# Performance work log

Hardware: AMD Instinct MI355X
Metric: run time of the kernel (lower is better)

The kernel has to match this reference:

```python
import jax, jax.numpy as jnp
import numpy as np

B, T, D, H = 4, 2048, 1024, 16
DK = D // H  # 64


def setup_inputs() -> dict:
    key = jax.random.key(0)
    ks = jax.random.split(key, 7)
    s = 1.0 / np.sqrt(D)
    x = jax.random.normal(ks[0], (B, T, D), dtype=jnp.float32)
    W_qkv = jax.random.normal(ks[1], (D, 3 * D), dtype=jnp.float32) * s
    b_qkv = jnp.zeros((3 * D,), dtype=jnp.float32)
    W_out = jax.random.normal(ks[2], (D, D), dtype=jnp.float32) * s
    b_out = jnp.zeros((D,), dtype=jnp.float32)
    # rotary tables: standard inv-freq construction, shape [T, DK//2]
    inv_freq = 1.0 / (10000.0 ** (np.arange(0, DK, 2, dtype=np.float32) / DK))
    ang = jnp.asarray(np.arange(T, dtype=np.float32)[:, None] * inv_freq[None, :])
    cos = jnp.cos(ang)
    sin = jnp.sin(ang)
    return {"x": x, "W_qkv": W_qkv, "b_qkv": b_qkv, "W_out": W_out,
            "b_out": b_out, "cos": cos, "sin": sin}


def _rope(t, cos, sin):
    # t: [B, H, T, DK]; cos/sin: [T, DK//2] broadcast over B, H
    t1, t2 = t[..., ::2], t[..., 1::2]
    return jnp.concatenate([t1 * cos - t2 * sin, t1 * sin + t2 * cos], axis=-1)


def reference(x, W_qkv, b_qkv, W_out, b_out, cos, sin):
    Bx, Tx, C = x.shape
    dk = C // H
    qkv = (x @ W_qkv + b_qkv).reshape(Bx, Tx, H, 3 * dk).transpose(0, 2, 1, 3)
    q, k, v = jnp.split(qkv, 3, axis=-1)  # each [B, H, T, dk]
    q = _rope(q, cos, sin)
    k = _rope(k, cos, sin)
    scores = jnp.einsum("bhtd,bhsd->bhts", q, k) / jnp.sqrt(jnp.float32(dk))
    causal = jnp.tril(jnp.ones((Tx, Tx), dtype=bool))  # [T, T]
    scores = jnp.where(causal, scores, jnp.float32(-jnp.inf))
    w = jax.nn.softmax(scores, axis=-1)  # dropout p=0.0 (eval): identity
    attn = jnp.einsum("bhts,bhsd->bhtd", w, v)
    attn = attn.transpose(0, 2, 1, 3).reshape(Bx, Tx, C)
    return attn @ W_out + b_out
```

## Files before the change

### kernel.cpp

```cpp
#include <hip/hip_runtime.h>
#include <cmath>

typedef __attribute__((ext_vector_type(4))) float f32x4;
typedef __attribute__((ext_vector_type(16))) float f32x16;
typedef __attribute__((ext_vector_type(8))) __bf16 bf16x8;
typedef __attribute__((ext_vector_type(8))) short s16x8;
typedef __attribute__((ext_vector_type(2))) unsigned int u32x2;

#define CB 4
#define CT 2048
#define CD 1024
#define CH 16
#define CDK 64
#define CBT 8192
#define CBH 64

#define GLOAD_LDS16(g, l)                                              \
  __builtin_amdgcn_global_load_lds(                                    \
      (const __attribute__((address_space(1))) unsigned int*)(g),      \
      (__attribute__((address_space(3))) unsigned int*)(l), 16, 0, 0)

__device__ __forceinline__ unsigned short f2bf(float f) {
  union { float f; unsigned u; } x; x.f = f;
  unsigned r = x.u + 0x7fffu + ((x.u >> 16) & 1u);
  return (unsigned short)(r >> 16);
}
__device__ __forceinline__ float bf2f(unsigned short b) {
  union { unsigned u; float f; } x; x.u = ((unsigned)b) << 16;
  return x.f;
}
__device__ __forceinline__ f32x4 mfma16(bf16x8 a, bf16x8 b, f32x4 c) {
  return __builtin_amdgcn_mfma_f32_16x16x32_bf16(a, b, c, 0, 0, 0);
}
__device__ __forceinline__ f32x16 mfma32(bf16x8 a, bf16x8 b, f32x16 c) {
  return __builtin_amdgcn_mfma_f32_32x32x16_bf16(a, b, c, 0, 0, 0);
}
__device__ __forceinline__ unsigned cvtpk(float lo, float hi) {
  unsigned r;
  asm("v_cvt_pk_bf16_f32 %0, %1, %2" : "=v"(r) : "v"(lo), "v"(hi));
  return r;
}

__global__ void convert_f32_bf16(const float* __restrict__ src,
                                 unsigned short* __restrict__ dst, int n) {
  int i = (blockIdx.x * blockDim.x + threadIdx.x) * 4;
  if (i >= n) return;
  float4 v = *(const float4*)(src + i);
  ushort4 o;
  o.x = f2bf(v.x); o.y = f2bf(v.y); o.z = f2bf(v.z); o.w = f2bf(v.w);
  *(ushort4*)(dst + i) = o;
}

__global__ void transpose_f32_bf16(const float* __restrict__ src,
                                   unsigned short* __restrict__ dst,
                                   int R, int C) {
  __shared__ float tile[32][33];
  const int x = threadIdx.x, y0 = threadIdx.y;
  const int ct = blockIdx.x, rt = blockIdx.y;
#pragma unroll
  for (int k = 0; k < 4; ++k) {
    int r = rt * 32 + y0 + k * 8;
    tile[y0 + k * 8][x] = src[(size_t)r * C + ct * 32 + x];
  }
  __syncthreads();
#pragma unroll
  for (int k = 0; k < 4; ++k) {
    int c = ct * 32 + y0 + k * 8;
    dst[(size_t)c * R + rt * 32 + x] = f2bf(tile[x][y0 + k * 8]);
  }
}

template <int MODE>
__global__ __launch_bounds__(256, 3) void gemm_bt(
    const unsigned short* __restrict__ A, const unsigned short* __restrict__ Bt,
    const float* __restrict__ bias, unsigned short* __restrict__ o0,
    unsigned short* __restrict__ o1, unsigned short* __restrict__ o2,
    float* __restrict__ fout, const float* __restrict__ cosT,
    const float* __restrict__ sinT, int M, int N, int K) {
  __shared__ __align__(16) unsigned short As[128 * 64];
  __shared__ __align__(16) unsigned short Bs[128 * 64];
  const int tid = threadIdx.x;
  const int lane = tid & 63, wid = tid >> 6;
  const int wr = wid >> 1, wc = wid & 1;
  const int m0 = blockIdx.x * 128, n0 = blockIdx.y * 128;
  const int l15 = lane & 15, l4 = lane >> 4;
  const int rx = l15 & 7;

  f32x4 acc[4][4];
#pragma unroll
  for (int i = 0; i < 4; ++i)
#pragma unroll
    for (int j = 0; j < 4; ++j) acc[i][j] = (f32x4){0.f, 0.f, 0.f, 0.f};

  const int srow = tid >> 3;
  const int scol = ((tid & 7) ^ (srow & 7)) * 8;
  const unsigned short* ag = A + (size_t)(m0 + srow) * K + scol;
  const unsigned short* bg = Bt + (size_t)(n0 + srow) * K + scol;
  unsigned short* asd = As + wid * 512;
  unsigned short* bsd = Bs + wid * 512;

  for (int k0 = 0; k0 < K; k0 += 64) {
#pragma unroll
    for (int p = 0; p < 4; ++p) {
      GLOAD_LDS16(ag + (size_t)(p * 32) * K + k0, asd + p * 2048);
      GLOAD_LDS16(bg + (size_t)(p * 32) * K + k0, bsd + p * 2048);
    }
    __syncthreads();
#pragma unroll
    for (int kk = 0; kk < 2; ++kk) {
      const int gsw = ((kk * 4 + l4) ^ rx) * 8;
      bf16x8 af[4], bfr[4];
#pragma unroll
      for (int i = 0; i < 4; ++i)
        af[i] = *(const bf16x8*)(&As[(wr * 64 + i * 16 + l15) * 64 + gsw]);
#pragma unroll
      for (int j = 0; j < 4; ++j)
        bfr[j] = *(const bf16x8*)(&Bs[(wc * 64 + j * 16 + l15) * 64 + gsw]);
#pragma unroll
      for (int i = 0; i < 4; ++i)
#pragma unroll
        for (int j = 0; j < 4; ++j)
          acc[i][j] = mfma16(af[i], bfr[j], acc[i][j]);
    }
    __syncthreads();
  }

  if (MODE == 1) {
#pragma unroll
    for (int i = 0; i < 4; ++i)
#pragma unroll
      for (int j = 0; j < 4; ++j) {
        const int row0 = m0 + wr * 64 + i * 16 + l4 * 4;
        const int col = n0 + wc * 64 + j * 16 + l15;
        const float bv = bias[col];
#pragma unroll
        for (int r = 0; r < 4; ++r)
          fout[(size_t)(row0 + r) * N + col] = acc[i][j][r] + bv;
      }
  } else {
#pragma unroll
    for (int i = 0; i < 4; ++i)
#pragma unroll
      for (int j = 0; j < 4; ++j) {
        const int col = n0 + wc * 64 + j * 16 + l15;
        const float bv = bias[col];
        const int h = col / 192;
        const int c = col % 192;
        const int sel = c >> 6;
        const int d = c & 63;
        if (sel < 2) {
          const int p = d >> 1;
          const bool even = (d & 1) == 0;
          const float qsc = (sel == 0) ? 0.18033688011112042592f : 1.0f;
          unsigned short* dst = (sel == 0) ? o0 : o1;
          const int dout = even ? p : (p + 32);
#pragma unroll
          for (int r = 0; r < 4; ++r) {
            const int row = m0 + wr * 64 + i * 16 + l4 * 4 + r;
            const int b = row >> 11, t = row & 2047;
            const float v = acc[i][j][r] + bv;
            const float vp = __shfl_xor(v, 1);
            const float cs = cosT[t * 32 + p];
            const float sn = sinT[t * 32 + p];
            const float ve = even ? v : vp;
            const float vo = even ? vp : v;
            const float res = (even ? (ve * cs - vo * sn)
                                    : (ve * sn + vo * cs)) * qsc;
            dst[((size_t)((b * CH + h) * CT + t)) * CDK + dout] = f2bf(res);
          }
        } else {
#pragma unroll
          for (int r = 0; r < 4; ++r) {
            const int row = m0 + wr * 64 + i * 16 + l4 * 4 + r;
            const int b = row >> 11, t = row & 2047;
            o2[((size_t)((b * CH + h) * CDK + d)) * CT + t] =
                f2bf(acc[i][j][r] + bv);
          }
        }
      }
  }
}

__global__ __launch_bounds__(256, 3) void attn_fwd4(
    const unsigned short* __restrict__ qg, const unsigned short* __restrict__ kg,
    const unsigned short* __restrict__ vtg, unsigned short* __restrict__ ctx) {
  __shared__ __align__(16) unsigned short Ks[3][64 * 64];
  __shared__ __align__(16) unsigned short Vt[3][64 * 64];
  const int tid = threadIdx.x, lane = tid & 63, w = tid >> 6;
  const int l31 = lane & 31, hi = lane >> 5;
  const int b1 = blockIdx.x;
  const int g8 = b1 & 7, idx8 = b1 >> 3;
  const int qb = 15 - (idx8 & 15);
  const int bh = g8 + 8 * (idx8 >> 4);
  const unsigned short* qp = qg + ((size_t)bh * CT + qb * 128) * CDK;
  const unsigned short* kp = kg + (size_t)bh * CT * CDK;
  const unsigned short* vp = vtg + (size_t)bh * CDK * CT;

  bf16x8 qf[4];
  {
    const unsigned short* qrow = qp + (size_t)(w * 32 + l31) * CDK + hi * 8;
#pragma unroll
    for (int ks = 0; ks < 4; ++ks) qf[ks] = *(const bf16x8*)(qrow + ks * 16);
  }
#pragma unroll
  for (int ks = 0; ks < 4; ++ks)
    asm volatile("" :: "v"(*(const f32x4*)&qf[ks]));

  const int lr = lane >> 3;
  const int gsw = ((lane & 7) ^ lr) * 8;
  const int row0 = w * 8 + lr;
  const unsigned short* ksrc0 = kp + (size_t)row0 * CDK + gsw;
  const unsigned short* ksrc1 = kp + (size_t)(row0 + 32) * CDK + gsw;
  const unsigned short* vsrc0 = vp + (size_t)row0 * CT + gsw;
  const unsigned short* vsrc1 = vp + (size_t)(row0 + 32) * CT + gsw;
  const int ld0 = w * 8 * 64;
  const int ld1 = (w * 8 + 32) * 64;

  const int NJ = 2 * qb + 2;
  const int njw = ((qb * 128 + w * 32 + 31) >> 6) + 1;
  const int qrow_g = qb * 128 + w * 32 + l31;

  auto STAGE = [&](int t, int buf) {
    const size_t koff = (size_t)t * 64 * CDK;
    const size_t voff = (size_t)t * 64;
    GLOAD_LDS16(ksrc0 + koff, &Ks[buf][ld0]);
    GLOAD_LDS16(ksrc1 + koff, &Ks[buf][ld1]);
    GLOAD_LDS16(vsrc0 + voff, &Vt[buf][ld0]);
    GLOAD_LDS16(vsrc1 + voff, &Vt[buf][ld1]);
  };

  f32x16 oacc[2];
#pragma unroll
  for (int nb = 0; nb < 2; ++nb)
#pragma unroll
    for (int r = 0; r < 16; ++r) oacc[nb][r] = 0.f;
  float lsum = 0.f;

  STAGE(0, 0);
  STAGE(1, 1);

  int b0 = 0;
  for (int j = 0; j < NJ; ++j) {
    int bp = b0 + 2; if (bp > 2) bp -= 3;
    if (j + 2 < NJ) STAGE(j + 2, bp);
    const int pend = NJ - 1 - j;
    if (pend >= 2)      asm volatile("s_waitcnt vmcnt(8)" ::: "memory");
    else if (pend == 1) asm volatile("s_waitcnt vmcnt(4)" ::: "memory");
    else                asm volatile("s_waitcnt vmcnt(0)" ::: "memory");
    __builtin_amdgcn_s_barrier();

    if (j < njw) {
      const unsigned short* KB = &Ks[b0][0];
      const unsigned short* VB = &Vt[b0][0];

      f32x16 pacc[2];
      __builtin_amdgcn_s_setprio(1);
#pragma unroll
      for (int kb = 0; kb < 2; ++kb) {
#pragma unroll
        for (int r = 0; r < 16; ++r) pacc[kb][r] = 0.f;
#pragma unroll
        for (int ks = 0; ks < 4; ++ks) {
          const int row = kb * 32 + l31;
          bf16x8 kf = *(const bf16x8*)(KB + row * 64 + (((ks * 2 + hi) ^ (row & 7)) * 8));
          pacc[kb] = mfma32(kf, qf[ks], pacc[kb]);
        }
      }
      __builtin_amdgcn_s_setprio(0);

      if (j == njw - 1) {
        const int key0 = j * 64;
#pragma unroll
        for (int kb = 0; kb < 2; ++kb)
#pragma unroll
          for (int r = 0; r < 16; ++r) {
            const int key = key0 + kb * 32 + (r & 3) + 8 * (r >> 2) + 4 * hi;
            if (key > qrow_g) pacc[kb][r] = -1e30f;
          }
      }

#pragma unroll
      for (int kb = 0; kb < 2; ++kb)
#pragma unroll
        for (int r = 0; r < 16; ++r)
          pacc[kb][r] = __builtin_amdgcn_exp2f(pacc[kb][r]);
      float rs;
      {
        float t[16];
#pragma unroll
        for (int r = 0; r < 16; ++r) t[r] = pacc[0][r] + pacc[1][r];
#pragma unroll
        for (int s = 8; s > 0; s >>= 1)
#pragma unroll
          for (int r = 0; r < s; ++r) t[r] += t[r + s];
        rs = t[0];
      }
      {
        unsigned ru = __float_as_uint(rs);
        u32x2 sw = __builtin_amdgcn_permlane32_swap(ru, ru, false, false);
        rs += __uint_as_float(hi ? sw[0] : sw[1]);
      }
      lsum += rs;

      bf16x8 pf[4];
#pragma unroll
      for (int kb = 0; kb < 2; ++kb)
#pragma unroll
        for (int half = 0; half < 2; ++half) {
          const int b0i = half * 8;
          unsigned c0 = cvtpk(pacc[kb][b0i + 0], pacc[kb][b0i + 1]);
          unsigned c1 = cvtpk(pacc[kb][b0i + 2], pacc[kb][b0i + 3]);
          unsigned c2 = cvtpk(pacc[kb][b0i + 4], pacc[kb][b0i + 5]);
          unsigned c3 = cvtpk(pacc[kb][b0i + 6], pacc[kb][b0i + 7]);
          u32x2 r02 = __builtin_amdgcn_permlane32_swap(c0, c2, false, false);
          u32x2 r13 = __builtin_amdgcn_permlane32_swap(c1, c3, false, false);
          union { unsigned u[4]; bf16x8 v; } fr;
          fr.u[0] = r02[0]; fr.u[1] = r13[0]; fr.u[2] = r02[1]; fr.u[3] = r13[1];
          pf[kb * 2 + half] = fr.v;
        }

      __builtin_amdgcn_s_setprio(1);
#pragma unroll
      for (int nb = 0; nb < 2; ++nb)
#pragma unroll
        for (int ks = 0; ks < 4; ++ks) {
          const int row = nb * 32 + l31;
          bf16x8 vf = *(const bf16x8*)(VB + row * 64 + (((ks * 2 + hi) ^ (row & 7)) * 8));
          oacc[nb] = mfma32(vf, pf[ks], oacc[nb]);
        }
      __builtin_amdgcn_s_setprio(0);
    }

    __builtin_amdgcn_s_barrier();
    b0 = (b0 == 2) ? 0 : b0 + 1;
  }

  __syncthreads();

  unsigned short* tr = &Ks[0][0] + w * 2048;
  const float inv = 1.f / lsum;
#pragma unroll
  for (int nb = 0; nb < 2; ++nb)
#pragma unroll
    for (int rp = 0; rp < 8; ++rp) {
      const int r = rp * 2;
      unsigned pkd = cvtpk(oacc[nb][r] * inv, oacc[nb][r + 1] * inv);
      const int d = nb * 32 + (r & 3) + 8 * (r >> 2) + 4 * hi;
      const int g = (d >> 3) ^ (l31 & 7);
      *(unsigned*)(tr + l31 * 64 + g * 8 + (d & 7)) = pkd;
    }
  const int b = bh >> 4, h = bh & 15;
#pragma unroll
  for (int s = 0; s < 4; ++s) {
    const int c = s * 64 + lane;
    const int qr = c >> 3, g = c & 7;
    s16x8 row = *(const s16x8*)(tr + qr * 64 + ((g ^ (qr & 7))) * 8);
    const int tok = qb * 128 + w * 32 + qr;
    *(s16x8*)(ctx + ((size_t)(b * CT + tok)) * CD + h * CDK + g * 8) = row;
  }
}

extern "C" void kernel_launch(void* const* d_in, const int* in_sizes, int n_in,
                              void* d_out, int out_size, void* d_ws, size_t ws_size,
                              hipStream_t stream) {
  (void)in_sizes; (void)n_in; (void)out_size; (void)ws_size;
  const float* x     = (const float*)d_in[0];
  const float* W_qkv = (const float*)d_in[1];
  const float* b_qkv = (const float*)d_in[2];
  const float* W_out = (const float*)d_in[3];
  const float* b_out = (const float*)d_in[4];
  const float* cosT  = (const float*)d_in[5];
  const float* sinT  = (const float*)d_in[6];
  float* out = (float*)d_out;

  unsigned short* xb   = (unsigned short*)d_ws;
  unsigned short* wqt  = xb + (size_t)CBT * CD;
  unsigned short* wot  = wqt + (size_t)3 * CD * CD;
  unsigned short* qbuf = wot + (size_t)CD * CD;
  unsigned short* kbuf = qbuf + (size_t)CBH * CT * CDK;
  unsigned short* vbuf = kbuf + (size_t)CBH * CT * CDK;
  unsigned short* ctx  = vbuf + (size_t)CBH * CT * CDK;

  {
    int n = CBT * CD;
    convert_f32_bf16<<<n / (256 * 4), 256, 0, stream>>>(x, xb, n);
  }
  transpose_f32_bf16<<<dim3(3 * CD / 32, CD / 32), dim3(32, 8), 0, stream>>>(
      W_qkv, wqt, CD, 3 * CD);
  transpose_f32_bf16<<<dim3(CD / 32, CD / 32), dim3(32, 8), 0, stream>>>(
      W_out, wot, CD, CD);
  gemm_bt<0><<<dim3(CBT / 128, 3 * CD / 128), 256, 0, stream>>>(
      xb, wqt, b_qkv, qbuf, kbuf, vbuf, nullptr, cosT, sinT, CBT, 3 * CD, CD);
  attn_fwd4<<<dim3(1024), 256, 0, stream>>>(qbuf, kbuf, vbuf, ctx);
  gemm_bt<1><<<dim3(CBT / 128, CD / 128), 256, 0, stream>>>(
      ctx, wot, b_out, nullptr, nullptr, nullptr, out, nullptr, nullptr,
      CBT, CD, CD);
}
```

Measured before the change: 172.8 us.

## Widen attention blocks to 256 query rows with 8 waves sharing K/V tiles

The attention kernel now runs 512 threads (8 waves) per block covering 256 query rows, so each staged 64-key K/V tile in LDS serves twice as many queries. Each thread issues one K and one V async load per stage instead of two each, and the vmcnt waits are halved to match. This cuts global K/V traffic and staging instructions per query. In exchange there are half as many blocks, the launch bound asks for 4 blocks/CU, and causal imbalance within a block grows, since early waves sit idle while later waves finish the diagonal tiles.

New measurement: 171.2 us. No clear change (-1.0%).

```diff
diff --git a/kernel.cpp b/kernel.cpp
--- a/kernel.cpp
+++ b/kernel.cpp
@@ -181,18 +181,19 @@
   }
 }
 
-__global__ __launch_bounds__(256, 3) void attn_fwd4(
+__global__ __launch_bounds__(512, 4) void attn_fwd5(
     const unsigned short* __restrict__ qg, const unsigned short* __restrict__ kg,
     const unsigned short* __restrict__ vtg, unsigned short* __restrict__ ctx) {
-  __shared__ __align__(16) unsigned short Ks[3][64 * 64];
-  __shared__ __align__(16) unsigned short Vt[3][64 * 64];
+  __shared__ __align__(16) unsigned short smem[24576];
+  unsigned short* Ks = smem;
+  unsigned short* Vt = smem + 12288;
   const int tid = threadIdx.x, lane = tid & 63, w = tid >> 6;
   const int l31 = lane & 31, hi = lane >> 5;
   const int b1 = blockIdx.x;
   const int g8 = b1 & 7, idx8 = b1 >> 3;
-  const int qb = 15 - (idx8 & 15);
-  const int bh = g8 + 8 * (idx8 >> 4);
-  const unsigned short* qp = qg + ((size_t)bh * CT + qb * 128) * CDK;
+  const int qb = 7 - (idx8 & 7);
+  const int bh = g8 + 8 * (idx8 >> 3);
+  const unsigned short* qp = qg + ((size_t)bh * CT + qb * 256) * CDK;
   const unsigned short* kp = kg + (size_t)bh * CT * CDK;
   const unsigned short* vp = vtg + (size_t)bh * CDK * CT;
 
@@ -207,26 +208,19 @@
     asm volatile("" :: "v"(*(const f32x4*)&qf[ks]));
 
   const int lr = lane >> 3;
+  const int srow = w * 8 + lr;
   const int gsw = ((lane & 7) ^ lr) * 8;
-  const int row0 = w * 8 + lr;
-  const unsigned short* ksrc0 = kp + (size_t)row0 * CDK + gsw;
-  const unsigned short* ksrc1 = kp + (size_t)(row0 + 32) * CDK + gsw;
-  const unsigned short* vsrc0 = vp + (size_t)row0 * CT + gsw;
-  const unsigned short* vsrc1 = vp + (size_t)(row0 + 32) * CT + gsw;
-  const int ld0 = w * 8 * 64;
-  const int ld1 = (w * 8 + 32) * 64;
-
-  const int NJ = 2 * qb + 2;
-  const int njw = ((qb * 128 + w * 32 + 31) >> 6) + 1;
-  const int qrow_g = qb * 128 + w * 32 + l31;
+  const unsigned short* ksrc = kp + (size_t)srow * CDK + gsw;
+  const unsigned short* vsrc = vp + (size_t)srow * CT + gsw;
+  const int ldo = w * 512;
+
+  const int NJ = 4 * qb + 4;
+  const int njw = ((qb * 256 + w * 32 + 31) >> 6) + 1;
+  const int qrow_g = qb * 256 + w * 32 + l31;
 
   auto STAGE = [&](int t, int buf) {
-    const size_t koff = (size_t)t * 64 * CDK;
-    const size_t voff = (size_t)t * 64;
-    GLOAD_LDS16(ksrc0 + koff, &Ks[buf][ld0]);
-    GLOAD_LDS16(ksrc1 + koff, &Ks[buf][ld1]);
-    GLOAD_LDS16(vsrc0 + voff, &Vt[buf][ld0]);
-    GLOAD_LDS16(vsrc1 + voff, &Vt[buf][ld1]);
+    GLOAD_LDS16(ksrc + (size_t)t * 64 * CDK, Ks + buf * 4096 + ldo);
+    GLOAD_LDS16(vsrc + (size_t)t * 64, Vt + buf * 4096 + ldo);
   };
 
   f32x16 oacc[2];
@@ -244,14 +238,14 @@
     int bp = b0 + 2; if (bp > 2) bp -= 3;
     if (j + 2 < NJ) STAGE(j + 2, bp);
     const int pend = NJ - 1 - j;
-    if (pend >= 2)      asm volatile("s_waitcnt vmcnt(8)" ::: "memory");
-    else if (pend == 1) asm volatile("s_waitcnt vmcnt(4)" ::: "memory");
+    if (pend >= 2)      asm volatile("s_waitcnt vmcnt(4)" ::: "memory");
+    else if (pend == 1) asm volatile("s_waitcnt vmcnt(2)" ::: "memory");
     else                asm volatile("s_waitcnt vmcnt(0)" ::: "memory");
     __builtin_amdgcn_s_barrier();
 
     if (j < njw) {
-      const unsigned short* KB = &Ks[b0][0];
-      const unsigned short* VB = &Vt[b0][0];
+      const unsigned short* KB = Ks + b0 * 4096;
+      const unsigned short* VB = Vt + b0 * 4096;
 
       f32x16 pacc[2];
       __builtin_amdgcn_s_setprio(1);
@@ -337,7 +331,7 @@
 
   __syncthreads();
 
-  unsigned short* tr = &Ks[0][0] + w * 2048;
+  unsigned short* tr = smem + w * 2048;
   const float inv = 1.f / lsum;
 #pragma unroll
   for (int nb = 0; nb < 2; ++nb)
@@ -355,7 +349,7 @@
     const int c = s * 64 + lane;
     const int qr = c >> 3, g = c & 7;
     s16x8 row = *(const s16x8*)(tr + qr * 64 + ((g ^ (qr & 7))) * 8);
-    const int tok = qb * 128 + w * 32 + qr;
+    const int tok = qb * 256 + w * 32 + qr;
     *(s16x8*)(ctx + ((size_t)(b * CT + tok)) * CD + h * CDK + g * 8) = row;
   }
 }
@@ -391,7 +385,7 @@
       W_out, wot, CD, CD);
   gemm_bt<0><<<dim3(CBT / 128, 3 * CD / 128), 256, 0, stream>>>(
       xb, wqt, b_qkv, qbuf, kbuf, vbuf, nullptr, cosT, sinT, CBT, 3 * CD, CD);
-  attn_fwd4<<<dim3(1024), 256, 0, stream>>>(qbuf, kbuf, vbuf, ctx);
+  attn_fwd5<<<dim3(512), 512, 0, stream>>>(qbuf, kbuf, vbuf, ctx);
   gemm_bt<1><<<dim3(CBT / 128, CD / 128), 256, 0, stream>>>(
       ctx, wot, b_out, nullptr, nullptr, nullptr, out, nullptr, nullptr,
       CBT, CD, CD);
```
